# Optimization experiments

Hardware: AMD Instinct MI355X
Metric: run time of the kernel (lower is better)

The kernel has to match this reference:

```python
import jax, jax.numpy as jnp
import numpy as np

D_MODEL = 1024
N_HEADS = 8
D_HEAD = 64
D_FF = 4096
LAMBDA_INIT = 0.8
EPS = 1e-5


def _ln(x, g, b):
    m = jnp.mean(x, axis=-1, keepdims=True)
    v = jnp.mean(jnp.square(x - m), axis=-1, keepdims=True)
    return (x - m) * jax.lax.rsqrt(v + EPS) * g + b


def setup_inputs() -> dict:
    key = jax.random.key(0)
    ks = jax.random.split(key, 24)
    D, H, Dh, F = D_MODEL, N_HEADS, D_HEAD, D_FF
    P = 2 * H * Dh  # projection width for q/k/v (== D here)
    s = lambda fan: 1.0 / np.sqrt(fan)
    inp = {
        'x': jax.random.normal(ks[0], (2, 2048, D), jnp.float32),
        'ln1_g': jnp.ones((D,), jnp.float32), 'ln1_b': jnp.zeros((D,), jnp.float32),
        'ln2_g': jnp.ones((D,), jnp.float32), 'ln2_b': jnp.zeros((D,), jnp.float32),
        'Wq': jax.random.normal(ks[1], (D, P), jnp.float32) * s(D), 'bq': jnp.zeros((P,), jnp.float32),
        'Wk': jax.random.normal(ks[2], (D, P), jnp.float32) * s(D), 'bk': jnp.zeros((P,), jnp.float32),
        'Wv': jax.random.normal(ks[3], (D, P), jnp.float32) * s(D), 'bv': jnp.zeros((P,), jnp.float32),
        'Wo': jax.random.normal(ks[4], (P, D), jnp.float32) * s(P), 'bo': jnp.zeros((D,), jnp.float32),
        'lq1': jax.random.normal(ks[5], (H, Dh), jnp.float32) * 0.1,
        'lk1': jax.random.normal(ks[6], (H, Dh), jnp.float32) * 0.1,
        'lq2': jax.random.normal(ks[7], (H, Dh), jnp.float32) * 0.1,
        'lk2': jax.random.normal(ks[8], (H, Dh), jnp.float32) * 0.1,
        'gn_w': jnp.ones((P,), jnp.float32), 'gn_b': jnp.zeros((P,), jnp.float32),
        'W1': jax.random.normal(ks[9], (D, F), jnp.float32) * s(D), 'b1': jnp.zeros((F,), jnp.float32),
        'Wg': jax.random.normal(ks[10], (F, F), jnp.float32) * s(F), 'bg': jnp.zeros((F,), jnp.float32),
        'W2': jax.random.normal(ks[11], (F, D), jnp.float32) * s(F), 'b2': jnp.zeros((D,), jnp.float32),
    }
    return inp


def reference(x, ln1_g, ln1_b, ln2_g, ln2_b, Wq, bq, Wk, bk, Wv, bv, Wo, bo,
              lq1, lk1, lq2, lk2, gn_w, gn_b, W1, b1, Wg, bg, W2, b2):
    B, S, D = x.shape
    H, Dh = N_HEADS, D_HEAD
    scale = 1.0 / np.sqrt(Dh)

    # --- differential attention sublayer (pre-norm) ---
    h = _ln(x, ln1_g, ln1_b)
    q = (h @ Wq + bq).reshape(B, S, H, 2, Dh)
    k = (h @ Wk + bk).reshape(B, S, H, 2, Dh)
    v = (h @ Wv + bv).reshape(B, S, H, 2 * Dh)

    A1 = jax.nn.softmax(jnp.einsum('bshd,bthd->bhst', q[..., 0, :], k[..., 0, :]) * scale, axis=-1)
    A2 = jax.nn.softmax(jnp.einsum('bshd,bthd->bhst', q[..., 1, :], k[..., 1, :]) * scale, axis=-1)

    lam = (jnp.exp(jnp.sum(lq1 * lk1, axis=-1))
           - jnp.exp(jnp.sum(lq2 * lk2, axis=-1)) + LAMBDA_INIT)  # [H]
    diff = A1 - lam[None, :, None, None] * A2                     # [B,H,S,S]
    o = jnp.einsum('bhst,bthe->bshe', diff, v)                    # [B,S,H,2*Dh]

    # headwise GroupNorm over the 2*Dh channels of each head
    mu = jnp.mean(o, axis=-1, keepdims=True)
    var = jnp.mean(jnp.square(o - mu), axis=-1, keepdims=True)
    o = (o - mu) * jax.lax.rsqrt(var + EPS)
    o = o * gn_w.reshape(H, 2 * Dh) + gn_b.reshape(H, 2 * Dh)
    o = o * (1.0 - LAMBDA_INIT)

    attn_out = o.reshape(B, S, 2 * H * Dh) @ Wo + bo
    x = x + attn_out

    # --- FFN sublayer: note source applies prenorm2 BEFORE residual split ---
    x = _ln(x, ln2_g, ln2_b)
    u = x @ W1 + b1
    u = u * jax.nn.silu(u @ Wg + bg)   # swiGLU gate
    return x + (u @ W2 + b2)
```

## Files before the change

### kernel.cpp

```cpp
#include <hip/hip_runtime.h>
#include <hip/hip_bf16.h>


typedef __attribute__((ext_vector_type(8))) __bf16 bf16x8;
typedef __attribute__((ext_vector_type(4))) float f32x4;

#define GAS __attribute__((address_space(1)))
#define LAS __attribute__((address_space(3)))

__device__ __forceinline__ unsigned short f2bf(float f) {
  unsigned u = __float_as_uint(f);
  u += 0x7fffu + ((u >> 16) & 1u);
  return (unsigned short)(u >> 16);
}
__device__ __forceinline__ float bf2f(unsigned short s) {
  return __uint_as_float(((unsigned)s) << 16);
}

__global__ __launch_bounds__(256)
void transpose_cvt(const float* __restrict__ W, unsigned short* __restrict__ WT,
                   int K, int N, float scale) {
  __shared__ float tile[64][65];
  const int n0 = blockIdx.x * 64, k0 = blockIdx.y * 64;
  const int tr = threadIdx.x >> 4, tc = (threadIdx.x & 15) * 4;
#pragma unroll
  for (int i = 0; i < 4; ++i) {
    const float4 v = *(const float4*)&W[(size_t)(k0 + tr + i * 16) * N + n0 + tc];
    tile[tr + i * 16][tc + 0] = v.x;
    tile[tr + i * 16][tc + 1] = v.y;
    tile[tr + i * 16][tc + 2] = v.z;
    tile[tr + i * 16][tc + 3] = v.w;
  }
  __syncthreads();
#pragma unroll
  for (int i = 0; i < 4; ++i) {
    const int n = tr + i * 16;
    ushort4 o;
    o.x = f2bf(tile[tc + 0][n] * scale);
    o.y = f2bf(tile[tc + 1][n] * scale);
    o.z = f2bf(tile[tc + 2][n] * scale);
    o.w = f2bf(tile[tc + 3][n] * scale);
    *(ushort4*)&WT[(size_t)(n0 + n) * K + k0 + tc] = o;
  }
}

__global__ void prep_bias(const float* __restrict__ bq, const float* __restrict__ bk,
                          const float* __restrict__ bv, float* __restrict__ out,
                          float qscale) {
  const int i = blockIdx.x * 256 + threadIdx.x;
  if (i < 1024) out[i] = bq[i] * qscale;
  else if (i < 2048) out[i] = bk[i - 1024];
  else out[i] = bv[i - 2048];
}

__global__ __launch_bounds__(256)
void k_pack(const unsigned short* __restrict__ qkv, unsigned short* __restrict__ KP) {
  const int bh = blockIdx.y, b = bh >> 3, h = bh & 7;
  const int s0 = blockIdx.x * 16;
  const int sl = threadIdx.x >> 4, e8 = (threadIdx.x & 15) * 8;
  const size_t src = (size_t)b * 2048 * 3072 + (size_t)(s0 + sl) * 3072 + 1024 + h * 128 + e8;
  const size_t dst = ((size_t)bh * 2048 + s0 + sl) * 128 + e8;
  *(uint4*)&KP[dst] = *(const uint4*)&qkv[src];
}

__global__ __launch_bounds__(256)
void v_transpose(const unsigned short* __restrict__ v, unsigned short* __restrict__ VT) {
  __shared__ unsigned short tile[64][65];
  const int s0 = blockIdx.x * 64, e0 = blockIdx.y * 64, bh = blockIdx.z;
  const int b = bh >> 3, h = bh & 7;
  const int tr = threadIdx.x >> 4, tc = (threadIdx.x & 15) * 4;
  const size_t inbase = (size_t)b * 2048 * 3072 + h * 128;
#pragma unroll
  for (int i = 0; i < 4; ++i) {
    const int r = tr + i * 16;
    const ushort4 val = *(const ushort4*)&v[inbase + (size_t)(s0 + r) * 3072 + e0 + tc];
    tile[r][tc + 0] = val.x;
    tile[r][tc + 1] = val.y;
    tile[r][tc + 2] = val.z;
    tile[r][tc + 3] = val.w;
  }
  __syncthreads();
#pragma unroll
  for (int i = 0; i < 4; ++i) {
    const int n = tr + i * 16;
    ushort4 oo;
    oo.x = tile[tc + 0][n];
    oo.y = tile[tc + 1][n];
    oo.z = tile[tc + 2][n];
    oo.w = tile[tc + 3][n];
    *(ushort4*)&VT[(size_t)(bh * 128 + e0 + n) * 2048 + s0 + tc] = oo;
  }
}

__global__ void lam_kernel(const float* __restrict__ lq1, const float* __restrict__ lk1,
                           const float* __restrict__ lq2, const float* __restrict__ lk2,
                           float* __restrict__ lam) {
  const int w = threadIdx.x >> 6, d = threadIdx.x & 63;
  float a = lq1[w * 64 + d] * lk1[w * 64 + d];
  float c = lq2[w * 64 + d] * lk2[w * 64 + d];
#pragma unroll
  for (int off = 32; off; off >>= 1) {
    a += __shfl_xor(a, off);
    c += __shfl_xor(c, off);
  }
  if (d == 0) lam[w] = __expf(a) - __expf(c) + 0.8f;
}

template <int WRITE_F32>
__global__ __launch_bounds__(256)
void ln_kernel(const float* __restrict__ x, const float* __restrict__ g,
               const float* __restrict__ bsh, unsigned short* __restrict__ obf,
               float* __restrict__ of32) {
  __shared__ float red[16];
  const int row = blockIdx.x, tid = threadIdx.x;
  const float4 v = *(const float4*)&x[(size_t)row * 1024 + tid * 4];
  float s = v.x + v.y + v.z + v.w;
  float q = v.x * v.x + v.y * v.y + v.z * v.z + v.w * v.w;
#pragma unroll
  for (int off = 32; off; off >>= 1) {
    s += __shfl_xor(s, off);
    q += __shfl_xor(q, off);
  }
  if ((tid & 63) == 0) {
    red[tid >> 6] = s;
    red[8 + (tid >> 6)] = q;
  }
  __syncthreads();
  s = red[0] + red[1] + red[2] + red[3];
  q = red[8] + red[9] + red[10] + red[11];
  const float mean = s * (1.f / 1024.f);
  const float var = q * (1.f / 1024.f) - mean * mean;
  const float rstd = rsqrtf(var + 1e-5f);
  const float4 gg = *(const float4*)&g[tid * 4];
  const float4 bb = *(const float4*)&bsh[tid * 4];
  float y0 = (v.x - mean) * rstd * gg.x + bb.x;
  float y1 = (v.y - mean) * rstd * gg.y + bb.y;
  float y2 = (v.z - mean) * rstd * gg.z + bb.z;
  float y3 = (v.w - mean) * rstd * gg.w + bb.w;
  const size_t base = (size_t)row * 1024 + tid * 4;
  ushort4 o;
  o.x = f2bf(y0); o.y = f2bf(y1); o.z = f2bf(y2); o.w = f2bf(y3);
  *(ushort4*)&obf[base] = o;
  if (WRITE_F32) {
    *(float4*)&of32[base] = make_float4(y0, y1, y2, y3);
  }
}

template <int EPI>
__global__ __launch_bounds__(256)
void gemm_n64(const unsigned short* __restrict__ A,
              const unsigned short* __restrict__ BT,
              const float* __restrict__ bias,
              const float* __restrict__ res,
              void* __restrict__ Cout, int M, int N, int K, float bscale) {
  __shared__ unsigned short ldsA[2][128 * 32];
  __shared__ unsigned short ldsB[2][64 * 32];
  const int tid = threadIdx.x;
  const int wv = tid >> 6, ln = tid & 63, lg = ln >> 4, lc = ln & 15;
  const int wm = wv >> 1, wn = wv & 1;
  const int nwg = gridDim.x * gridDim.y;
  const int linear = blockIdx.y * gridDim.x + blockIdx.x;
  const int swz = (linear & 7) * (nwg >> 3) + (linear >> 3);
  const int m0 = (swz / gridDim.x) * 128, n0 = (swz % gridDim.x) * 64;
  const int rsub = ln >> 2;
  const int sw_inner = ((ln & 3) * 16) ^ ((rsub & 3) << 4);
  const int acol = sw_inner >> 1;

  f32x4 acc[4][2];
#pragma unroll
  for (int i = 0; i < 4; ++i)
#pragma unroll
    for (int j = 0; j < 2; ++j) acc[i][j] = (f32x4)0.f;

  auto stage = [&](int buf, int k0) {
#pragma unroll
    for (int j = 0; j < 2; ++j) {
      const int rowblk = wv * 32 + j * 16;
      const unsigned short* ga = A + (size_t)(m0 + rowblk + rsub) * K + (k0 + acol);
      __builtin_amdgcn_global_load_lds((GAS void*)ga,
          (LAS void*)&ldsA[buf][rowblk * 32], 16, 0, 0);
    }
    const unsigned short* gb = BT + (size_t)(n0 + wv * 16 + rsub) * K + (k0 + acol);
    __builtin_amdgcn_global_load_lds((GAS void*)gb,
        (LAS void*)&ldsB[buf][wv * 16 * 32], 16, 0, 0);
  };

  const int nk = K / 32;
  stage(0, 0);
  int cur = 0;
  for (int i = 0; i < nk; ++i) {
    if (i + 1 < nk) {
      stage(cur ^ 1, (i + 1) * 32);
      asm volatile("s_waitcnt vmcnt(3)" ::: "memory");
    } else {
      asm volatile("s_waitcnt vmcnt(0)" ::: "memory");
    }
    __builtin_amdgcn_s_barrier();
    bf16x8 af[4], bf[2];
#pragma unroll
    for (int m = 0; m < 4; ++m) {
      const int r = wm * 64 + m * 16 + lc;
      af[m] = *(const bf16x8*)((const char*)&ldsA[cur][0] + r * 64 +
                               ((lg * 16) ^ ((r & 3) << 4)));
    }
#pragma unroll
    for (int n = 0; n < 2; ++n) {
      const int r = wn * 32 + n * 16 + lc;
      bf[n] = *(const bf16x8*)((const char*)&ldsB[cur][0] + r * 64 +
                               ((lg * 16) ^ ((r & 3) << 4)));
    }
    __builtin_amdgcn_s_setprio(1);
#pragma unroll
    for (int m = 0; m < 4; ++m)
#pragma unroll
      for (int n = 0; n < 2; ++n)
        acc[m][n] = __builtin_amdgcn_mfma_f32_16x16x32_bf16(af[m], bf[n], acc[m][n], 0, 0, 0);
    __builtin_amdgcn_s_setprio(0);
    __builtin_amdgcn_s_barrier();
    cur ^= 1;
  }

#pragma unroll
  for (int m = 0; m < 4; ++m) {
#pragma unroll
    for (int n = 0; n < 2; ++n) {
      const int c = n0 + wn * 32 + n * 16 + lc;
      const float bc = bias[c] * bscale;
#pragma unroll
      for (int j = 0; j < 4; ++j) {
        const int r = m0 + wm * 64 + m * 16 + lg * 4 + j;
        const size_t idx = (size_t)r * N + c;
        const float v = acc[m][n][j] + bc;
        if (EPI == 1) {
          ((float*)Cout)[idx] = res[idx] + v;
        } else {
          ((unsigned short*)Cout)[idx] = f2bf(v);
        }
      }
    }
  }
}

template <int EPI>
__global__ __launch_bounds__(512)
void gemm256(const unsigned short* __restrict__ A,
             const unsigned short* __restrict__ BT,
             const float* __restrict__ bias,
             const unsigned short* __restrict__ gate_u,
             unsigned short* __restrict__ Cout, int M, int N, int K) {
  __shared__ unsigned short lds[65536];
  const int tid = threadIdx.x;
  const int w = tid >> 6, ln = tid & 63, lg = ln >> 4, lc = ln & 15;
  const int wm = w >> 2, wn = w & 3;
  const int nwg = gridDim.x * gridDim.y;
  const int linear = blockIdx.y * gridDim.x + blockIdx.x;
  const int swzb = (linear & 7) * (nwg >> 3) + (linear >> 3);
  const int m0 = (swzb / gridDim.x) * 256, n0 = (swzb % gridDim.x) * 256;

  f32x4 acc[8][4];
#pragma unroll
  for (int i = 0; i < 8; ++i)
#pragma unroll
    for (int j = 0; j < 4; ++j) acc[i][j] = (f32x4)0.f;

  auto stage_half = [&](int tensor, int j, int hh) {
    const unsigned short* base = tensor ? BT : A;
    const int row0 = (tensor ? n0 : m0) + hh * 128;
    const int slot = tensor * 4 + (j & 1) * 2 + hh;
#pragma unroll
    for (int c = 0; c < 2; ++c) {
      const int chunk = w * 2 + c;
      const int L = chunk * 1024 + ln * 16;
      const int r = L >> 7, inner = L & 127;
      const char* src = (const char*)(base + (size_t)(row0 + r) * K + j * 64) +
                        (inner ^ ((r & 7) << 4));
      __builtin_amdgcn_global_load_lds((GAS void*)src,
          (LAS void*)((char*)lds + slot * 16384 + chunk * 1024), 16, 0, 0);
    }
  };
  auto read_a = [&](int j, int mf, int ks) -> bf16x8 {
    const int r = mf * 16 + lc;
    const int slot = (j & 1) * 2 + wm;
    const int cb = ks * 64 + lg * 16;
    return *(const bf16x8*)((const char*)lds + slot * 16384 + r * 128 +
                            (cb ^ ((r & 7) << 4)));
  };
  auto read_b = [&](int j, int nf, int ks) -> bf16x8 {
    const int R = wn * 64 + nf * 16 + lc;
    const int slot = 4 + (j & 1) * 2 + (R >> 7);
    const int r = R & 127;
    const int cb = ks * 64 + lg * 16;
    return *(const bf16x8*)((const char*)lds + slot * 16384 + r * 128 +
                            (cb ^ ((r & 7) << 4)));
  };

  const int nkt = K / 64;

  stage_half(0, 0, 0); stage_half(0, 0, 1);
  stage_half(1, 0, 0); stage_half(1, 0, 1);
  stage_half(1, 1, 0); stage_half(1, 1, 1);
  asm volatile("s_waitcnt vmcnt(0)" ::: "memory");
  __builtin_amdgcn_s_barrier();

  bf16x8 bfr[4][2];
  for (int it = 0; it < nkt / 2; ++it) {
    const int J = it * 2;
#pragma unroll
    for (int half = 0; half < 2; ++half) {
      const int jc = J + half;
#pragma unroll
      for (int q = 0; q < 4; ++q) {
        if (q == 0) {
#pragma unroll
          for (int nf = 0; nf < 4; ++nf)
#pragma unroll
            for (int ks = 0; ks < 2; ++ks) bfr[nf][ks] = read_b(jc, nf, ks);
        }
        bf16x8 afr[2][2];
#pragma unroll
        for (int mm = 0; mm < 2; ++mm)
#pragma unroll
          for (int ks = 0; ks < 2; ++ks) afr[mm][ks] = read_a(jc, q * 2 + mm, ks);
        if (half == 0) {
          if (q == 0) stage_half(0, J + 1, 0);
          if (q == 1) stage_half(0, J + 1, 1);
          if (q == 2 && J + 2 < nkt) stage_half(1, J + 2, 0);
          if (q == 3 && J + 2 < nkt) stage_half(1, J + 2, 1);
        } else {
          if (q == 0 && J + 2 < nkt) stage_half(0, J + 2, 0);
          if (q == 1 && J + 2 < nkt) stage_half(0, J + 2, 1);
          if (q == 2 && J + 3 < nkt) stage_half(1, J + 3, 0);
          if (q == 3 && J + 3 < nkt) stage_half(1, J + 3, 1);
        }
        if (q == 0) asm volatile("s_waitcnt lgkmcnt(8)" ::: "memory");
        if (q == 3) asm volatile("s_waitcnt vmcnt(4)" ::: "memory");
        __builtin_amdgcn_s_barrier();
        __builtin_amdgcn_s_setprio(1);
#pragma unroll
        for (int mm = 0; mm < 2; ++mm)
#pragma unroll
          for (int nf = 0; nf < 4; ++nf)
#pragma unroll
            for (int ks = 0; ks < 2; ++ks)
              acc[q * 2 + mm][nf] = __builtin_amdgcn_mfma_f32_16x16x32_bf16(
                  afr[mm][ks], bfr[nf][ks], acc[q * 2 + mm][nf], 0, 0, 0);
        __builtin_amdgcn_s_setprio(0);
        __builtin_amdgcn_s_barrier();
      }
    }
  }

#pragma unroll
  for (int mf = 0; mf < 8; ++mf) {
#pragma unroll
    for (int nf = 0; nf < 4; ++nf) {
      const int c = n0 + wn * 64 + nf * 16 + lc;
      const float bc = bias[c];
#pragma unroll
      for (int jj = 0; jj < 4; ++jj) {
        const int r = m0 + wm * 128 + mf * 16 + lg * 4 + jj;
        const size_t idx = (size_t)r * N + c;
        const float v = acc[mf][nf][jj] + bc;
        if (EPI == 0) {
          Cout[idx] = f2bf(v);
        } else {
          const float uu = bf2f(gate_u[idx]);
          const float sw = v / (1.f + __expf(-v));
          Cout[idx] = f2bf(uu * sw);
        }
      }
    }
  }
}

__global__ __launch_bounds__(256)
void attn_kernel(const unsigned short* __restrict__ q,
                 const unsigned short* __restrict__ KP,
                 const unsigned short* __restrict__ VT,
                 float* __restrict__ Opart,
                 float* __restrict__ lsumPart) {
  constexpr int S = 2048;
  constexpr int QS = 3072;
  __shared__ unsigned short k_tile[2][32 * 128];
  __shared__ unsigned short v_tile[2][128 * 32];
  __shared__ unsigned short p_lds[4][2][512];
  const int tid = threadIdx.x, w = tid >> 6, ln = tid & 63, lg = ln >> 4, lc = ln & 15;
  const int id = blockIdx.x;
  const int bh = (id & 7) + 8 * ((id >> 9) & 1);
  const int qt = (id >> 3) & 31;
  const int tcn = (id >> 8) & 1;
  const size_t chan = (size_t)(bh >> 3) * S * QS + (bh & 7) * 128;
  const size_t kpbase = (size_t)bh * S * 128;
  const size_t vtbase = (size_t)bh * 128 * S;
  const int qrow = qt * 64 + w * 16 + lc;

  bf16x8 qf[2][2];
#pragma unroll
  for (int p = 0; p < 2; ++p)
#pragma unroll
    for (int ks = 0; ks < 2; ++ks)
      qf[p][ks] = *(const bf16x8*)&q[chan + (size_t)qrow * QS + p * 64 + ks * 32 + lg * 8];

  f32x4 O[2][8];
#pragma unroll
  for (int p = 0; p < 2; ++p)
#pragma unroll
    for (int ef = 0; ef < 8; ++ef) O[p][ef] = (f32x4)0.f;
  float lsum[2][4];
#pragma unroll
  for (int p = 0; p < 2; ++p)
#pragma unroll
    for (int j = 0; j < 4; ++j) lsum[p][j] = 0.f;

  const int prd = ((lc * 64 + lg * 16) ^ ((lc & 7) << 4)) >> 1;

  auto stage = [&](int buf, int t0) {
#pragma unroll
    for (int c = 0; c < 2; ++c) {
      {
        const int L = (w * 2 + c) * 1024 + ln * 16;
        const int r = L >> 8, inner = L & 255;
        const char* src = (const char*)(KP + kpbase + (size_t)(t0 + r) * 128) +
                          (inner ^ ((r & 7) << 4));
        __builtin_amdgcn_global_load_lds((GAS void*)src,
            (LAS void*)((char*)&k_tile[buf][0] + (w * 2 + c) * 1024), 16, 0, 0);
      }
      {
        const int L = (w * 2 + c) * 1024 + ln * 16;
        const int e = L >> 6, inner = L & 63;
        const char* src = (const char*)(VT + vtbase + (size_t)e * S + t0) +
                          (inner ^ ((e & 3) << 4));
        __builtin_amdgcn_global_load_lds((GAS void*)src,
            (LAS void*)((char*)&v_tile[buf][0] + (w * 2 + c) * 1024), 16, 0, 0);
      }
    }
  };

  auto compute = [&](int buf) {
    const char* kb = (const char*)&k_tile[buf][0];
    const char* vb = (const char*)&v_tile[buf][0];
    bf16x8 vf[8];
#pragma unroll
    for (int ef = 0; ef < 8; ++ef) {
      const int e = ef * 16 + lc;
      vf[ef] = *(const bf16x8*)(vb + e * 64 + ((lg * 16) ^ ((e & 3) << 4)));
    }
#pragma unroll
    for (int p = 0; p < 2; ++p) {
      bf16x8 kf[2][2];
#pragma unroll
      for (int tf = 0; tf < 2; ++tf) {
        const int r = tf * 16 + lc;
#pragma unroll
        for (int ks = 0; ks < 2; ++ks)
          kf[tf][ks] = *(const bf16x8*)(kb + r * 256 +
                          ((p * 128 + ks * 64 + lg * 16) ^ ((r & 7) << 4)));
      }
      f32x4 sfr[2];
      __builtin_amdgcn_s_setprio(1);
#pragma unroll
      for (int tf = 0; tf < 2; ++tf) {
        f32x4 acc = (f32x4)0.f;
#pragma unroll
        for (int ks = 0; ks < 2; ++ks)
          acc = __builtin_amdgcn_mfma_f32_16x16x32_bf16(qf[p][ks], kf[tf][ks], acc, 0, 0, 0);
        sfr[tf] = acc;
      }
      __builtin_amdgcn_s_setprio(0);

#pragma unroll
      for (int tf = 0; tf < 2; ++tf)
#pragma unroll
        for (int j = 0; j < 4; ++j) {
          const float e = __expf(sfr[tf][j]);
          lsum[p][j] += e;
          const int qq = lg * 4 + j;
          const int wi = ((qq * 64 + (tf * 16 + lc) * 2) ^ ((qq & 7) << 4)) >> 1;
          p_lds[w][p][wi] = f2bf(e);
        }

      const bf16x8 pa = *(const bf16x8*)&p_lds[w][p][prd];
      __builtin_amdgcn_s_setprio(1);
#pragma unroll
      for (int ef = 0; ef < 8; ++ef)
        O[p][ef] = __builtin_amdgcn_mfma_f32_16x16x32_bf16(pa, vf[ef], O[p][ef], 0, 0, 0);
      __builtin_amdgcn_s_setprio(0);
    }
  };

  const int tbeg = tcn * (S / 2);
  stage(0, tbeg);
  int cur = 0;
  for (int it = 0; it < 32; ++it) {
    if (it < 31) {
      stage(cur ^ 1, tbeg + (it + 1) * 32);
      asm volatile("s_waitcnt vmcnt(4)" ::: "memory");
    } else {
      asm volatile("s_waitcnt vmcnt(0)" ::: "memory");
    }
    __builtin_amdgcn_s_barrier();
    compute(cur);
    __builtin_amdgcn_s_barrier();
    cur ^= 1;
  }

  const size_t rowbase = ((size_t)tcn * 16 + bh) * S;
#pragma unroll
  for (int p = 0; p < 2; ++p)
#pragma unroll
    for (int j = 0; j < 4; ++j) {
      float s = lsum[p][j];
      s += __shfl_xor(s, 1);
      s += __shfl_xor(s, 2);
      s += __shfl_xor(s, 4);
      s += __shfl_xor(s, 8);
      const int row = qt * 64 + w * 16 + lg * 4 + j;
      if (lc == 0)
        lsumPart[(rowbase + row) * 2 + p] = s;
#pragma unroll
      for (int ef = 0; ef < 8; ++ef)
        Opart[(rowbase + row) * 256 + p * 128 + ef * 16 + lc] = O[p][ef][j];
    }
}

__global__ __launch_bounds__(256)
void attn_reduce(const float* __restrict__ Opart, const float* __restrict__ lsumPart,
                 const float* __restrict__ lam,
                 const float* __restrict__ gn_w, const float* __restrict__ gn_b,
                 unsigned short* __restrict__ o) {
  constexpr int S = 2048;
  const int gw = (blockIdx.x * 256 + threadIdx.x) >> 6;
  const int ln = threadIdx.x & 63;
  const int bh = gw >> 11, s = gw & 2047;
  const int b = bh >> 3, h = bh & 7;
  const size_t r0 = ((size_t)bh * S + s) * 256;
  const size_t r1 = (((size_t)16 + bh) * S + s) * 256;
  const int e = ln * 2;
  const float2 o1a = *(const float2*)&Opart[r0 + e];
  const float2 o1b = *(const float2*)&Opart[r1 + e];
  const float2 o2a = *(const float2*)&Opart[r0 + 128 + e];
  const float2 o2b = *(const float2*)&Opart[r1 + 128 + e];
  const size_t l0 = ((size_t)bh * S + s) * 2;
  const size_t l1 = (((size_t)16 + bh) * S + s) * 2;
  const float inv1 = 1.f / (lsumPart[l0] + lsumPart[l1]);
  const float inv2 = lam[h] / (lsumPart[l0 + 1] + lsumPart[l1 + 1]);
  float d0 = (o1a.x + o1b.x) * inv1 - (o2a.x + o2b.x) * inv2;
  float d1 = (o1a.y + o1b.y) * inv1 - (o2a.y + o2b.y) * inv2;
  float sum = d0 + d1, sq = d0 * d0 + d1 * d1;
#pragma unroll
  for (int off = 32; off; off >>= 1) {
    sum += __shfl_xor(sum, off);
    sq += __shfl_xor(sq, off);
  }
  const float mean = sum * (1.f / 128.f);
  const float var = sq * (1.f / 128.f) - mean * mean;
  const float rstd = rsqrtf(var + 1e-5f);
  const float v0 = ((d0 - mean) * rstd * gn_w[h * 128 + e] + gn_b[h * 128 + e]) * 0.2f;
  const float v1 = ((d1 - mean) * rstd * gn_w[h * 128 + e + 1] + gn_b[h * 128 + e + 1]) * 0.2f;
  ushort2 ov;
  ov.x = f2bf(v0);
  ov.y = f2bf(v1);
  *(ushort2*)&o[(size_t)b * S * 1024 + (size_t)s * 1024 + h * 128 + e] = ov;
}

extern "C" void kernel_launch(void* const* d_in, const int* in_sizes, int n_in,
                              void* d_out, int out_size, void* d_ws, size_t ws_size,
                              hipStream_t stream) {
  (void)in_sizes; (void)n_in; (void)out_size; (void)ws_size;
  const float* x    = (const float*)d_in[0];
  const float* ln1g = (const float*)d_in[1];
  const float* ln1b = (const float*)d_in[2];
  const float* ln2g = (const float*)d_in[3];
  const float* ln2b = (const float*)d_in[4];
  const float* Wq   = (const float*)d_in[5];
  const float* bq   = (const float*)d_in[6];
  const float* Wk   = (const float*)d_in[7];
  const float* bk   = (const float*)d_in[8];
  const float* Wv   = (const float*)d_in[9];
  const float* bv   = (const float*)d_in[10];
  const float* Wo   = (const float*)d_in[11];
  const float* bo   = (const float*)d_in[12];
  const float* lq1  = (const float*)d_in[13];
  const float* lk1  = (const float*)d_in[14];
  const float* lq2  = (const float*)d_in[15];
  const float* lk2  = (const float*)d_in[16];
  const float* gnw  = (const float*)d_in[17];
  const float* gnb  = (const float*)d_in[18];
  const float* W1   = (const float*)d_in[19];
  const float* b1   = (const float*)d_in[20];
  const float* Wg   = (const float*)d_in[21];
  const float* bg   = (const float*)d_in[22];
  const float* W2   = (const float*)d_in[23];
  const float* b2   = (const float*)d_in[24];

  const int B = 2, S = 2048, D = 1024, F = 4096;
  const int M = B * S;
  const float qscale = 0.125f;

  char* ws = (char*)d_ws;
  size_t off = 0;
  auto alloc = [&](size_t bytes) {
    char* p = ws + off;
    off += (bytes + 255) & ~(size_t)255;
    return p;
  };
  unsigned short* WqkvT = (unsigned short*)alloc((size_t)3 * D * D * 2);
  unsigned short* WoT = (unsigned short*)alloc((size_t)D * D * 2);
  unsigned short* W1T = (unsigned short*)alloc((size_t)F * D * 2);
  unsigned short* WgT = (unsigned short*)alloc((size_t)F * F * 2);
  unsigned short* W2T = (unsigned short*)alloc((size_t)D * F * 2);
  float*          lamw= (float*)alloc(256);
  float*          bqkv= (float*)alloc(3072 * 4);
  unsigned short* h_bf= (unsigned short*)alloc((size_t)M * D * 2);
  unsigned short* qkv = (unsigned short*)alloc((size_t)M * 3 * D * 2);
  unsigned short* o_bf= (unsigned short*)alloc((size_t)M * D * 2);
  float*          x1  = (float*)alloc((size_t)M * D * 4);
  float*          x2  = (float*)alloc((size_t)M * D * 4);
  unsigned short* x2b = (unsigned short*)alloc((size_t)M * D * 2);
  unsigned short* u_bf= (unsigned short*)alloc((size_t)M * F * 2);
  float*          lsumP = (float*)alloc((size_t)2 * 16 * S * 2 * 4);
  unsigned short* w_bf= h_bf;

  float* Opart = (float*)x1;
  unsigned short* VT = u_bf + (size_t)12 * 1024 * 1024;
  unsigned short* KP = o_bf;

  transpose_cvt<<<dim3(D / 64, D / 64), 256, 0, stream>>>(Wq, WqkvT, D, D, qscale);
  transpose_cvt<<<dim3(D / 64, D / 64), 256, 0, stream>>>(Wk, WqkvT + (size_t)D * D, D, D, 1.0f);
  transpose_cvt<<<dim3(D / 64, D / 64), 256, 0, stream>>>(Wv, WqkvT + (size_t)2 * D * D, D, D, 1.0f);
  transpose_cvt<<<dim3(D / 64, D / 64), 256, 0, stream>>>(Wo, WoT, D, D, 1.0f);
  transpose_cvt<<<dim3(F / 64, D / 64), 256, 0, stream>>>(W1, W1T, D, F, 1.0f);
  transpose_cvt<<<dim3(F / 64, F / 64), 256, 0, stream>>>(Wg, WgT, F, F, 1.0f);
  transpose_cvt<<<dim3(D / 64, F / 64), 256, 0, stream>>>(W2, W2T, F, D, 1.0f);
  prep_bias<<<12, 256, 0, stream>>>(bq, bk, bv, bqkv, qscale);
  lam_kernel<<<1, 512, 0, stream>>>(lq1, lk1, lq2, lk2, lamw);

  ln_kernel<0><<<M, 256, 0, stream>>>(x, ln1g, ln1b, h_bf, nullptr);
  gemm256<0><<<dim3(3 * D / 256, M / 256), 512, 0, stream>>>(h_bf, WqkvT, bqkv, nullptr, qkv, M, 3 * D, D);
  k_pack<<<dim3(S / 16, 16), 256, 0, stream>>>(qkv, KP);
  v_transpose<<<dim3(S / 64, 2, 16), 256, 0, stream>>>(qkv + 2048, VT);
  attn_kernel<<<dim3(1024), 256, 0, stream>>>(qkv, KP, VT, Opart, lsumP);
  attn_reduce<<<dim3(8192), 256, 0, stream>>>(Opart, lsumP, lamw, gnw, gnb, o_bf);
  gemm_n64<1><<<dim3(D / 64, M / 128), 256, 0, stream>>>(o_bf, WoT, bo, x, x1, M, D, D, 1.0f);

  ln_kernel<1><<<M, 256, 0, stream>>>(x1, ln2g, ln2b, x2b, x2);
  gemm256<0><<<dim3(F / 256, M / 256), 512, 0, stream>>>(x2b, W1T, b1, nullptr, u_bf, M, F, D);
  gemm256<2><<<dim3(F / 256, M / 256), 512, 0, stream>>>(u_bf, WgT, bg, u_bf, w_bf, M, F, F);
  gemm_n64<1><<<dim3(D / 64, M / 128), 256, 0, stream>>>(w_bf, W2T, b2, x2, (float*)d_out, M, D, F, 1.0f);
}
```

Measured before the change: 464.4 us.

## Fuse attention split-K reduce and GroupNorm into attention kernel epilogue

Removes the two-way key split in the attention kernel so each block covers the full sequence, then performs softmax normalization, the lambda-weighted difference, headwise GroupNorm and the bf16 store directly in the epilogue. This drops the fp32 partial-output round trip through global memory and the separate reduce launch, at the cost of halving the grid to 512 blocks and doubling per-block loop length, which can reduce occupancy and parallelism. It also moves a vmcnt wait in the GEMM to after the MFMA block so the load wait overlaps compute.

```diff
diff --git a/kernel.cpp b/kernel.cpp
--- a/kernel.cpp
+++ b/kernel.cpp
@@ -333,7 +333,6 @@
           if (q == 3 && J + 3 < nkt) stage_half(1, J + 3, 1);
         }
         if (q == 0) asm volatile("s_waitcnt lgkmcnt(8)" ::: "memory");
-        if (q == 3) asm volatile("s_waitcnt vmcnt(4)" ::: "memory");
         __builtin_amdgcn_s_barrier();
         __builtin_amdgcn_s_setprio(1);
 #pragma unroll
@@ -345,6 +344,7 @@
               acc[q * 2 + mm][nf] = __builtin_amdgcn_mfma_f32_16x16x32_bf16(
                   afr[mm][ks], bfr[nf][ks], acc[q * 2 + mm][nf], 0, 0, 0);
         __builtin_amdgcn_s_setprio(0);
+        if (q == 3) asm volatile("s_waitcnt vmcnt(4)" ::: "memory");
         __builtin_amdgcn_s_barrier();
       }
     }
@@ -377,8 +377,9 @@
 void attn_kernel(const unsigned short* __restrict__ q,
                  const unsigned short* __restrict__ KP,
                  const unsigned short* __restrict__ VT,
-                 float* __restrict__ Opart,
-                 float* __restrict__ lsumPart) {
+                 const float* __restrict__ lam,
+                 const float* __restrict__ gn_w, const float* __restrict__ gn_b,
+                 unsigned short* __restrict__ o) {
   constexpr int S = 2048;
   constexpr int QS = 3072;
   __shared__ unsigned short k_tile[2][32 * 128];
@@ -386,10 +387,11 @@
   __shared__ unsigned short p_lds[4][2][512];
   const int tid = threadIdx.x, w = tid >> 6, ln = tid & 63, lg = ln >> 4, lc = ln & 15;
   const int id = blockIdx.x;
-  const int bh = (id & 7) + 8 * ((id >> 9) & 1);
+  const int bh = (id & 7) + 8 * ((id >> 8) & 1);
   const int qt = (id >> 3) & 31;
-  const int tcn = (id >> 8) & 1;
-  const size_t chan = (size_t)(bh >> 3) * S * QS + (bh & 7) * 128;
+  const int h = bh & 7, b = bh >> 3;
+  const size_t chan = (size_t)b * S * QS + h * 128;
+  const size_t ochan = (size_t)b * S * 1024 + h * 128;
   const size_t kpbase = (size_t)bh * S * 128;
   const size_t vtbase = (size_t)bh * 128 * S;
   const int qrow = qt * 64 + w * 16 + lc;
@@ -488,12 +490,11 @@
     }
   };
 
-  const int tbeg = tcn * (S / 2);
-  stage(0, tbeg);
+  stage(0, 0);
   int cur = 0;
-  for (int it = 0; it < 32; ++it) {
-    if (it < 31) {
-      stage(cur ^ 1, tbeg + (it + 1) * 32);
+  for (int it = 0; it < 64; ++it) {
+    if (it < 63) {
+      stage(cur ^ 1, (it + 1) * 32);
       asm volatile("s_waitcnt vmcnt(4)" ::: "memory");
     } else {
       asm volatile("s_waitcnt vmcnt(0)" ::: "memory");
@@ -504,7 +505,6 @@
     cur ^= 1;
   }
 
-  const size_t rowbase = ((size_t)tcn * 16 + bh) * S;
 #pragma unroll
   for (int p = 0; p < 2; ++p)
 #pragma unroll
@@ -514,53 +514,35 @@
       s += __shfl_xor(s, 2);
       s += __shfl_xor(s, 4);
       s += __shfl_xor(s, 8);
-      const int row = qt * 64 + w * 16 + lg * 4 + j;
-      if (lc == 0)
-        lsumPart[(rowbase + row) * 2 + p] = s;
-#pragma unroll
-      for (int ef = 0; ef < 8; ++ef)
-        Opart[(rowbase + row) * 256 + p * 128 + ef * 16 + lc] = O[p][ef][j];
-    }
-}
-
-__global__ __launch_bounds__(256)
-void attn_reduce(const float* __restrict__ Opart, const float* __restrict__ lsumPart,
-                 const float* __restrict__ lam,
-                 const float* __restrict__ gn_w, const float* __restrict__ gn_b,
-                 unsigned short* __restrict__ o) {
-  constexpr int S = 2048;
-  const int gw = (blockIdx.x * 256 + threadIdx.x) >> 6;
-  const int ln = threadIdx.x & 63;
-  const int bh = gw >> 11, s = gw & 2047;
-  const int b = bh >> 3, h = bh & 7;
-  const size_t r0 = ((size_t)bh * S + s) * 256;
-  const size_t r1 = (((size_t)16 + bh) * S + s) * 256;
-  const int e = ln * 2;
-  const float2 o1a = *(const float2*)&Opart[r0 + e];
-  const float2 o1b = *(const float2*)&Opart[r1 + e];
-  const float2 o2a = *(const float2*)&Opart[r0 + 128 + e];
-  const float2 o2b = *(const float2*)&Opart[r1 + 128 + e];
-  const size_t l0 = ((size_t)bh * S + s) * 2;
-  const size_t l1 = (((size_t)16 + bh) * S + s) * 2;
-  const float inv1 = 1.f / (lsumPart[l0] + lsumPart[l1]);
-  const float inv2 = lam[h] / (lsumPart[l0 + 1] + lsumPart[l1 + 1]);
-  float d0 = (o1a.x + o1b.x) * inv1 - (o2a.x + o2b.x) * inv2;
-  float d1 = (o1a.y + o1b.y) * inv1 - (o2a.y + o2b.y) * inv2;
-  float sum = d0 + d1, sq = d0 * d0 + d1 * d1;
-#pragma unroll
-  for (int off = 32; off; off >>= 1) {
-    sum += __shfl_xor(sum, off);
-    sq += __shfl_xor(sq, off);
-  }
-  const float mean = sum * (1.f / 128.f);
-  const float var = sq * (1.f / 128.f) - mean * mean;
-  const float rstd = rsqrtf(var + 1e-5f);
-  const float v0 = ((d0 - mean) * rstd * gn_w[h * 128 + e] + gn_b[h * 128 + e]) * 0.2f;
-  const float v1 = ((d1 - mean) * rstd * gn_w[h * 128 + e + 1] + gn_b[h * 128 + e + 1]) * 0.2f;
-  ushort2 ov;
-  ov.x = f2bf(v0);
-  ov.y = f2bf(v1);
-  *(ushort2*)&o[(size_t)b * S * 1024 + (size_t)s * 1024 + h * 128 + e] = ov;
+      lsum[p][j] = s;
+    }
+  const float lamh = lam[h];
+#pragma unroll
+  for (int j = 0; j < 4; ++j) {
+    const float inv1 = 1.f / lsum[0][j];
+    const float inv2 = lamh / lsum[1][j];
+    float dv[8], sum = 0.f, sq = 0.f;
+#pragma unroll
+    for (int ef = 0; ef < 8; ++ef) {
+      dv[ef] = O[0][ef][j] * inv1 - O[1][ef][j] * inv2;
+      sum += dv[ef];
+      sq += dv[ef] * dv[ef];
+    }
+    sum += __shfl_xor(sum, 1); sq += __shfl_xor(sq, 1);
+    sum += __shfl_xor(sum, 2); sq += __shfl_xor(sq, 2);
+    sum += __shfl_xor(sum, 4); sq += __shfl_xor(sq, 4);
+    sum += __shfl_xor(sum, 8); sq += __shfl_xor(sq, 8);
+    const float mean = sum * (1.f / 128.f);
+    const float var = sq * (1.f / 128.f) - mean * mean;
+    const float rstd = rsqrtf(var + 1e-5f);
+    const int row = qt * 64 + w * 16 + lg * 4 + j;
+#pragma unroll
+    for (int ef = 0; ef < 8; ++ef) {
+      const int e = ef * 16 + lc;
+      const float val = (dv[ef] - mean) * rstd * gn_w[h * 128 + e] + gn_b[h * 128 + e];
+      o[ochan + (size_t)row * 1024 + e] = f2bf(val * 0.2f);
+    }
+  }
 }
 
 extern "C" void kernel_launch(void* const* d_in, const int* in_sizes, int n_in,
@@ -618,12 +600,10 @@
   float*          x2  = (float*)alloc((size_t)M * D * 4);
   unsigned short* x2b = (unsigned short*)alloc((size_t)M * D * 2);
   unsigned short* u_bf= (unsigned short*)alloc((size_t)M * F * 2);
-  float*          lsumP = (float*)alloc((size_t)2 * 16 * S * 2 * 4);
   unsigned short* w_bf= h_bf;
 
-  float* Opart = (float*)x1;
+  unsigned short* KP = (unsigned short*)x1;
   unsigned short* VT = u_bf + (size_t)12 * 1024 * 1024;
-  unsigned short* KP = o_bf;
 
   transpose_cvt<<<dim3(D / 64, D / 64), 256, 0, stream>>>(Wq, WqkvT, D, D, qscale);
   transpose_cvt<<<dim3(D / 64, D / 64), 256, 0, stream>>>(Wk, WqkvT + (size_t)D * D, D, D, 1.0f);
@@ -639,8 +619,7 @@
   gemm256<0><<<dim3(3 * D / 256, M / 256), 512, 0, stream>>>(h_bf, WqkvT, bqkv, nullptr, qkv, M, 3 * D, D);
   k_pack<<<dim3(S / 16, 16), 256, 0, stream>>>(qkv, KP);
   v_transpose<<<dim3(S / 64, 2, 16), 256, 0, stream>>>(qkv + 2048, VT);
-  attn_kernel<<<dim3(1024), 256, 0, stream>>>(qkv, KP, VT, Opart, lsumP);
-  attn_reduce<<<dim3(8192), 256, 0, stream>>>(Opart, lsumP, lamw, gnw, gnb, o_bf);
+  attn_kernel<<<dim3(512), 256, 0, stream>>>(qkv, KP, VT, lamw, gnw, gnb, o_bf);
   gemm_n64<1><<<dim3(D / 64, M / 128), 256, 0, stream>>>(o_bf, WoT, bo, x, x1, M, D, D, 1.0f);
 
   ln_kernel<1><<<M, 256, 0, stream>>>(x1, ln2g, ln2b, x2b, x2);
```

Result: faster. 451.6 us (-2.8%).
